# Kernel tuning notes

Hardware: AMD Instinct MI355X
Metric: run time of the kernel (lower is better)

The kernel has to match this reference:

```python
import jax, jax.numpy as jnp
import numpy as np

B, S, D, H = 2, 4096, 1024, 16
HD = D // H  # 64
BASE = 10000.0


def setup_inputs() -> dict:
    key = jax.random.key(0)
    ks = jax.random.split(key, 11)
    s = 1.0 / np.sqrt(D)
    return {
        "consulta": jax.random.normal(ks[0], (B, S, D), jnp.float32),
        "chave": jax.random.normal(ks[1], (B, S, D), jnp.float32),
        "valor": jax.random.normal(ks[2], (B, S, D), jnp.float32),
        "Wq": jax.random.normal(ks[3], (D, D), jnp.float32) * s,
        "bq": jnp.zeros((D,), jnp.float32),
        "Wk": jax.random.normal(ks[4], (D, D), jnp.float32) * s,
        "bk": jnp.zeros((D,), jnp.float32),
        "Wv": jax.random.normal(ks[5], (D, D), jnp.float32) * s,
        "bv": jnp.zeros((D,), jnp.float32),
        "Wo": jax.random.normal(ks[6], (D, D), jnp.float32) * s,
        "bo": jnp.zeros((D,), jnp.float32),
    }


def _rope(x):
    # x: [B, H, S, HD]; rotate interleaved (even, odd) pairs
    seq = x.shape[2]
    theta = 1.0 / (BASE ** (jnp.arange(0, HD, 2, dtype=jnp.float32) / HD))  # [HD/2]
    angles = jnp.arange(seq, dtype=jnp.float32)[:, None] * theta[None, :]  # [S, HD/2]
    cos, sin = jnp.cos(angles), jnp.sin(angles)
    xr = x.reshape(*x.shape[:-1], HD // 2, 2)
    x_re, x_im = xr[..., 0], xr[..., 1]
    out_re = x_re * cos - x_im * sin
    out_im = x_re * sin + x_im * cos
    return jnp.stack([out_re, out_im], axis=-1).reshape(x.shape)


def reference(consulta, chave, valor, Wq, bq, Wk, bk, Wv, bv, Wo, bo):
    b, s, _ = consulta.shape
    # projections (torch Linear: x @ W.T + b)
    Q = consulta @ Wq.T + bq
    K = chave @ Wk.T + bk
    V = valor @ Wv.T + bv
    # [B, H, S, HD]
    Q = Q.reshape(b, s, H, HD).transpose(0, 2, 1, 3)
    K = K.reshape(b, s, H, HD).transpose(0, 2, 1, 3)
    V = V.reshape(b, s, H, HD).transpose(0, 2, 1, 3)
    Q = _rope(Q)
    K = _rope(K)
    scores = jnp.einsum('bhqd,bhkd->bhqk', Q, K) / jnp.sqrt(jnp.float32(HD))
    weights = jax.nn.softmax(scores, axis=-1)  # dropout p=0 -> identity
    out = jnp.einsum('bhqk,bhkd->bhqd', weights, V)
    out = out.transpose(0, 2, 1, 3).reshape(b, s, D)
    return out @ Wo.T + bo
```

## Files before the change

kernel.cpp:

```cpp
#include <hip/hip_runtime.h>
#include <hip/hip_bf16.h>

typedef __attribute__((ext_vector_type(8))) short short8;
typedef __attribute__((ext_vector_type(4))) float f32x4;
typedef __attribute__((ext_vector_type(4))) unsigned short ushort4v;
typedef __attribute__((ext_vector_type(4))) float float4v;

#define NB 2
#define NS 4096
#define ND 1024
#define NH 16
#define NHD 64

__device__ __forceinline__ unsigned short f2bf(float x) {
    union { float f; unsigned u; } v; v.f = x;
    unsigned r = v.u + 0x7FFFu + ((v.u >> 16) & 1u);
    return (unsigned short)(r >> 16);
}
__device__ __forceinline__ float bf2f(unsigned short u) {
    union { float f; unsigned u; } v; v.u = ((unsigned)u) << 16;
    return v.f;
}

__device__ __forceinline__ void gload_lds16(const unsigned short* g, unsigned short* l) {
    __builtin_amdgcn_global_load_lds(
        (const __attribute__((address_space(1))) void*)g,
        (__attribute__((address_space(3))) void*)l,
        16, 0, 0);
}

__global__ void rope_table_kernel(float* __restrict__ cosT, float* __restrict__ sinT) {
    int i = blockIdx.x * blockDim.x + threadIdx.x;
    int p = i & 31, s = i >> 5;
    float theta = exp2f(-(float)(2 * p) * (13.287712379549449f / 64.0f));
    float ang = (float)s * theta;
    float sv, cv;
    sincosf(ang, &sv, &cv);
    cosT[i] = cv; sinT[i] = sv;
}

__global__ void cast_bf16_kernel(const float* __restrict__ in, unsigned short* __restrict__ out, int n8) {
    int i = blockIdx.x * blockDim.x + threadIdx.x;
    if (i >= n8) return;
    float4v a0 = *(const float4v*)(&in[(size_t)i * 8]);
    float4v a1 = *(const float4v*)(&in[(size_t)i * 8 + 4]);
    short8 s8;
    s8[0] = (short)f2bf(a0.x); s8[1] = (short)f2bf(a0.y);
    s8[2] = (short)f2bf(a0.z); s8[3] = (short)f2bf(a0.w);
    s8[4] = (short)f2bf(a1.x); s8[5] = (short)f2bf(a1.y);
    s8[6] = (short)f2bf(a1.z); s8[7] = (short)f2bf(a1.w);
    *(short8*)(&out[(size_t)i * 8]) = s8;
}

template<int EPI>
__global__ __launch_bounds__(256, 2) void gemm_kernel(
    const unsigned short* __restrict__ A,
    const unsigned short* __restrict__ Wb,
    const float* __restrict__ bias,
    void* __restrict__ outv,
    const float* __restrict__ cosT,
    const float* __restrict__ sinT)
{
    __shared__ unsigned short As[128 * 32];
    __shared__ unsigned short Bs[128 * 32];
    const int t = threadIdx.x;
    const int wave = t >> 6, lane = t & 63;
    const int quad = lane >> 4, l15 = lane & 15;
    const int wm = (wave & 1) * 64, wn = (wave >> 1) * 64;
    const int m0 = blockIdx.y * 128, n0 = blockIdx.x * 128;

    f32x4 acc[4][4];
#pragma unroll
    for (int i = 0; i < 4; i++)
#pragma unroll
        for (int j = 0; j < 4; j++)
            acc[i][j] = f32x4{0.f, 0.f, 0.f, 0.f};

    for (int k0 = 0; k0 < ND; k0 += 32) {
#pragma unroll
        for (int p = 0; p < 2; p++) {
            int idx = p * 256 + t;
            int r = idx >> 2, c = (idx & 3) * 8;
            unsigned short* ldsA = &As[(size_t)(p * 256 + wave * 64) * 8];
            unsigned short* ldsB = &Bs[(size_t)(p * 256 + wave * 64) * 8];
            gload_lds16(&A[(size_t)(m0 + r) * ND + k0 + c], ldsA);
            gload_lds16(&Wb[(size_t)(n0 + r) * ND + k0 + c], ldsB);
        }
        __syncthreads();

        short8 af[4], bfr[4];
#pragma unroll
        for (int mt = 0; mt < 4; mt++)
            af[mt] = *(const short8*)(&As[(wm + mt * 16 + l15) * 32 + quad * 8]);
#pragma unroll
        for (int nt = 0; nt < 4; nt++)
            bfr[nt] = *(const short8*)(&Bs[(wn + nt * 16 + l15) * 32 + quad * 8]);
#pragma unroll
        for (int mt = 0; mt < 4; mt++)
#pragma unroll
            for (int nt = 0; nt < 4; nt++) {
                if (EPI == 0)
                    acc[mt][nt] = __builtin_amdgcn_mfma_f32_16x16x32_bf16(bfr[nt], af[mt], acc[mt][nt], 0, 0, 0);
                else
                    acc[mt][nt] = __builtin_amdgcn_mfma_f32_16x16x32_bf16(af[mt], bfr[nt], acc[mt][nt], 0, 0, 0);
            }
        __syncthreads();
    }

    if (EPI == 0) {
        float* out = (float*)outv;
#pragma unroll
        for (int mt = 0; mt < 4; mt++) {
            int gm = m0 + wm + mt * 16 + l15;
#pragma unroll
            for (int nt = 0; nt < 4; nt++) {
                int gn0 = n0 + wn + nt * 16 + quad * 4;
                float4v fv;
#pragma unroll
                for (int r = 0; r < 4; r++)
                    fv[r] = acc[mt][nt][r] + bias[gn0 + r];
                *(float4v*)(&out[(size_t)gm * ND + gn0]) = fv;
            }
        }
    } else if (EPI == 1) {
        unsigned short* out = (unsigned short*)outv;
#pragma unroll
        for (int nt = 0; nt < 4; nt++) {
            int gn = n0 + wn + nt * 16 + l15;
            int h = gn >> 6, hd = gn & 63, pr = hd >> 1, im = gn & 1;
            float bv = bias[gn];
#pragma unroll
            for (int mt = 0; mt < 4; mt++) {
                int gm0 = m0 + wm + mt * 16 + quad * 4;
#pragma unroll
                for (int r = 0; r < 4; r++) {
                    int gm = gm0 + r;
                    int b = gm >> 12, s = gm & 4095;
                    float v = acc[mt][nt][r] + bv;
                    float pv = __shfl_xor(v, 1, 64);
                    float cv = cosT[s * 32 + pr], sv = sinT[s * 32 + pr];
                    float o = im ? (pv * sv + v * cv) : (v * cv - pv * sv);
                    out[((size_t)(b * NH + h) * NS + s) * NHD + hd] = f2bf(o);
                }
            }
        }
    } else {
        unsigned short* out = (unsigned short*)outv;
#pragma unroll
        for (int nt = 0; nt < 4; nt++) {
            int gn = n0 + wn + nt * 16 + l15;
            int h = gn >> 6, hd = gn & 63;
            float bv = bias[gn];
#pragma unroll
            for (int mt = 0; mt < 4; mt++) {
                int gm0 = m0 + wm + mt * 16 + quad * 4;
                int b = gm0 >> 12, s0 = gm0 & 4095;
                ushort4v pk;
#pragma unroll
                for (int r = 0; r < 4; r++)
                    pk[r] = f2bf(acc[mt][nt][r] + bv);
                *(ushort4v*)(&out[((size_t)(b * NH + h) * NHD + hd) * NS + s0]) = pk;
            }
        }
    }
}

__global__ __launch_bounds__(256, 2) void flash_kernel(
    const unsigned short* __restrict__ Qr,
    const unsigned short* __restrict__ Kr,
    const unsigned short* __restrict__ Vt,
    unsigned short* __restrict__ Yatt)
{
    __shared__ unsigned short Ks[128 * 72];
    __shared__ unsigned short Vs[64 * 136];
    __shared__ unsigned short Pw[4][32 * 136];
    const int t = threadIdx.x;
    const int wave = t >> 6, lane = t & 63;
    const int quad = lane >> 4, l15 = lane & 15;
    const int bh = blockIdx.y;
    const int qb = blockIdx.x * 128;
    const int wq = wave * 32;
    const size_t base = (size_t)bh * NS * NHD;

    short8 qf[2][2];
#pragma unroll
    for (int nt = 0; nt < 2; nt++)
#pragma unroll
        for (int kk = 0; kk < 2; kk++)
            qf[nt][kk] = *(const short8*)(&Qr[base + (size_t)(qb + wq + nt * 16 + l15) * NHD + kk * 32 + quad * 8]);

    f32x4 accO[4][2];
#pragma unroll
    for (int i = 0; i < 4; i++)
#pragma unroll
        for (int j = 0; j < 2; j++)
            accO[i][j] = f32x4{0.f, 0.f, 0.f, 0.f};
    float mrow[2] = {-1e30f, -1e30f};
    float lrow[2] = {0.f, 0.f};

    for (int j0 = 0; j0 < NS; j0 += 128) {
#pragma unroll
        for (int p = 0; p < 4; p++) {
            int idx = p * 256 + t;
            { int r = idx >> 3, c = (idx & 7) * 8;
              *(short8*)(&Ks[r * 72 + c]) = *(const short8*)(&Kr[base + (size_t)(j0 + r) * NHD + c]); }
            { int r = idx >> 4, c = (idx & 15) * 8;
              *(short8*)(&Vs[r * 136 + c]) = *(const short8*)(&Vt[(size_t)(bh * NHD + r) * NS + j0 + c]); }
        }
        __syncthreads();

        f32x4 sa[8][2];
#pragma unroll
        for (int mt = 0; mt < 8; mt++)
#pragma unroll
            for (int nt = 0; nt < 2; nt++)
                sa[mt][nt] = f32x4{0.f, 0.f, 0.f, 0.f};
#pragma unroll
        for (int kk = 0; kk < 2; kk++)
#pragma unroll
            for (int mt = 0; mt < 8; mt++) {
                short8 ak = *(const short8*)(&Ks[(mt * 16 + l15) * 72 + kk * 32 + quad * 8]);
#pragma unroll
                for (int nt = 0; nt < 2; nt++)
                    sa[mt][nt] = __builtin_amdgcn_mfma_f32_16x16x32_bf16(ak, qf[nt][kk], sa[mt][nt], 0, 0, 0);
            }

#pragma unroll
        for (int nt = 0; nt < 2; nt++) {
            float mx = -1e30f;
#pragma unroll
            for (int mt = 0; mt < 8; mt++)
#pragma unroll
                for (int r = 0; r < 4; r++)
                    mx = fmaxf(mx, sa[mt][nt][r]);
            mx = fmaxf(mx, __shfl_xor(mx, 16, 64));
            mx = fmaxf(mx, __shfl_xor(mx, 32, 64));
            mx *= 0.125f;
            float mnew = fmaxf(mrow[nt], mx);
            float alpha = __expf(mrow[nt] - mnew);
            float lsum = 0.f;
#pragma unroll
            for (int mt = 0; mt < 8; mt++) {
                ushort4v pk;
#pragma unroll
                for (int r = 0; r < 4; r++) {
                    float pv = __expf(sa[mt][nt][r] * 0.125f - mnew);
                    unsigned short u = f2bf(pv);
                    pk[r] = u;
                    lsum += bf2f(u);
                }
                *(ushort4v*)(&Pw[wave][(nt * 16 + l15) * 136 + mt * 16 + quad * 4]) = pk;
            }
            lsum += __shfl_xor(lsum, 16, 64);
            lsum += __shfl_xor(lsum, 32, 64);
            lrow[nt] = lrow[nt] * alpha + lsum;
            mrow[nt] = mnew;
#pragma unroll
            for (int mt2 = 0; mt2 < 4; mt2++)
#pragma unroll
                for (int r = 0; r < 4; r++)
                    accO[mt2][nt][r] *= alpha;
        }
        __syncthreads();

#pragma unroll
        for (int kk2 = 0; kk2 < 4; kk2++) {
            short8 av[4], bp[2];
#pragma unroll
            for (int mt2 = 0; mt2 < 4; mt2++)
                av[mt2] = *(const short8*)(&Vs[(mt2 * 16 + l15) * 136 + kk2 * 32 + quad * 8]);
#pragma unroll
            for (int nt = 0; nt < 2; nt++)
                bp[nt] = *(const short8*)(&Pw[wave][(nt * 16 + l15) * 136 + kk2 * 32 + quad * 8]);
#pragma unroll
            for (int mt2 = 0; mt2 < 4; mt2++)
#pragma unroll
                for (int nt = 0; nt < 2; nt++)
                    accO[mt2][nt] = __builtin_amdgcn_mfma_f32_16x16x32_bf16(av[mt2], bp[nt], accO[mt2][nt], 0, 0, 0);
        }
        __syncthreads();
    }

    int b = bh >> 4, h = bh & 15;
#pragma unroll
    for (int nt = 0; nt < 2; nt++) {
        float rl = 1.f / lrow[nt];
        int s = qb + wq + nt * 16 + l15;
#pragma unroll
        for (int mt2 = 0; mt2 < 4; mt2++) {
            ushort4v pk;
#pragma unroll
            for (int r = 0; r < 4; r++)
                pk[r] = f2bf(accO[mt2][nt][r] * rl);
            *(ushort4v*)(&Yatt[((size_t)(b * NS + s)) * ND + h * NHD + mt2 * 16 + quad * 4]) = pk;
        }
    }
}

extern "C" void kernel_launch(void* const* d_in, const int* in_sizes, int n_in,
                              void* d_out, int out_size, void* d_ws, size_t ws_size,
                              hipStream_t stream) {
    const float* consulta = (const float*)d_in[0];
    const float* chave    = (const float*)d_in[1];
    const float* valor    = (const float*)d_in[2];
    const float* Wq = (const float*)d_in[3];
    const float* bq = (const float*)d_in[4];
    const float* Wk = (const float*)d_in[5];
    const float* bk = (const float*)d_in[6];
    const float* Wv = (const float*)d_in[7];
    const float* bv = (const float*)d_in[8];
    const float* Wo = (const float*)d_in[9];
    const float* bo = (const float*)d_in[10];

    const size_t NX = (size_t)8192 * 1024;

    float* cosT = (float*)d_ws;
    float* sinT = cosT + (size_t)NS * 32;
    unsigned short* Qrb = (unsigned short*)(sinT + (size_t)NS * 32);
    unsigned short* Krb = Qrb + NX;
    unsigned short* Vtb = Krb + NX;
    unsigned short* Yat = Vtb + NX;
    unsigned short* Abf = Yat + NX;
    unsigned short* Wbf = Abf + NX;

    rope_table_kernel<<<NS * 32 / 256, 256, 0, stream>>>(cosT, sinT);

    const int ACT8 = (int)(NX / 8);
    const int W8 = ND * ND / 8;

    dim3 ggrid(8, 64);

    cast_bf16_kernel<<<ACT8 / 256, 256, 0, stream>>>(consulta, Abf, ACT8);
    cast_bf16_kernel<<<W8 / 256, 256, 0, stream>>>(Wq, Wbf, W8);
    gemm_kernel<1><<<ggrid, 256, 0, stream>>>(Abf, Wbf, bq, Qrb, cosT, sinT);

    cast_bf16_kernel<<<ACT8 / 256, 256, 0, stream>>>(chave, Abf, ACT8);
    cast_bf16_kernel<<<W8 / 256, 256, 0, stream>>>(Wk, Wbf, W8);
    gemm_kernel<1><<<ggrid, 256, 0, stream>>>(Abf, Wbf, bk, Krb, cosT, sinT);

    cast_bf16_kernel<<<ACT8 / 256, 256, 0, stream>>>(valor, Abf, ACT8);
    cast_bf16_kernel<<<W8 / 256, 256, 0, stream>>>(Wv, Wbf, W8);
    gemm_kernel<2><<<ggrid, 256, 0, stream>>>(Abf, Wbf, bv, Vtb, cosT, sinT);

    flash_kernel<<<dim3(32, 32), 256, 0, stream>>>(Qrb, Krb, Vtb, Yat);

    cast_bf16_kernel<<<W8 / 256, 256, 0, stream>>>(Wo, Wbf, W8);
    gemm_kernel<0><<<ggrid, 256, 0, stream>>>(Yat, Wbf, bo, d_out, cosT, sinT);
}
```

Measured before the change: 560.3 us.

## Fold softmax scale into Q, use exp2, per-tile P buffer, raise flash occupancy

Folds the 1/sqrt(d) and log2(e) factors into the Q projection epilogue, so the flash kernel can use exp2 directly without a per-score multiply. The P buffer now holds one 16-row tile per wave, and the PV MFMAs run inside the per-nt softmax loop. This halves P shared memory and allows launch_bounds of 3 blocks per CU. It also uses packed v_cvt_pk_bf16 conversion and tree max/sum reductions, at the cost of a row sum taken over unrounded fp32 P values, which differs slightly from the bf16 values fed to the MFMA.

```diff
diff --git a/kernel.cpp b/kernel.cpp
--- a/kernel.cpp
+++ b/kernel.cpp
@@ -5,6 +5,7 @@
 typedef __attribute__((ext_vector_type(4))) float f32x4;
 typedef __attribute__((ext_vector_type(4))) unsigned short ushort4v;
 typedef __attribute__((ext_vector_type(4))) float float4v;
+typedef __attribute__((ext_vector_type(2))) unsigned int uint32x2;
 
 #define NB 2
 #define NS 4096
@@ -12,14 +13,18 @@
 #define NH 16
 #define NHD 64
 
+#define QSCALE 0.18033688011112042f
+
 __device__ __forceinline__ unsigned short f2bf(float x) {
     union { float f; unsigned u; } v; v.f = x;
     unsigned r = v.u + 0x7FFFu + ((v.u >> 16) & 1u);
     return (unsigned short)(r >> 16);
 }
-__device__ __forceinline__ float bf2f(unsigned short u) {
-    union { float f; unsigned u; } v; v.u = ((unsigned)u) << 16;
-    return v.f;
+
+__device__ __forceinline__ unsigned cvt_pk_bf16(float lo, float hi) {
+    unsigned r;
+    asm("v_cvt_pk_bf16_f32 %0, %1, %2" : "=v"(r) : "v"(lo), "v"(hi));
+    return r;
 }
 
 __device__ __forceinline__ void gload_lds16(const unsigned short* g, unsigned short* l) {
@@ -59,7 +64,8 @@
     const float* __restrict__ bias,
     void* __restrict__ outv,
     const float* __restrict__ cosT,
-    const float* __restrict__ sinT)
+    const float* __restrict__ sinT,
+    float oscale)
 {
     __shared__ unsigned short As[128 * 32];
     __shared__ unsigned short Bs[128 * 32];
@@ -140,7 +146,7 @@
                     float pv = __shfl_xor(v, 1, 64);
                     float cv = cosT[s * 32 + pr], sv = sinT[s * 32 + pr];
                     float o = im ? (pv * sv + v * cv) : (v * cv - pv * sv);
-                    out[((size_t)(b * NH + h) * NS + s) * NHD + hd] = f2bf(o);
+                    out[((size_t)(b * NH + h) * NS + s) * NHD + hd] = f2bf(o * oscale);
                 }
             }
         }
@@ -165,7 +171,7 @@
     }
 }
 
-__global__ __launch_bounds__(256, 2) void flash_kernel(
+__global__ __launch_bounds__(256, 3) void flash_kernel(
     const unsigned short* __restrict__ Qr,
     const unsigned short* __restrict__ Kr,
     const unsigned short* __restrict__ Vt,
@@ -173,7 +179,7 @@
 {
     __shared__ unsigned short Ks[128 * 72];
     __shared__ unsigned short Vs[64 * 136];
-    __shared__ unsigned short Pw[4][32 * 136];
+    __shared__ unsigned short Pw[4][16 * 136];
     const int t = threadIdx.x;
     const int wave = t >> 6, lane = t & 63;
     const int quad = lane >> 4, l15 = lane & 15;
@@ -227,30 +233,31 @@
 
 #pragma unroll
         for (int nt = 0; nt < 2; nt++) {
-            float mx = -1e30f;
+            float mm[8];
 #pragma unroll
             for (int mt = 0; mt < 8; mt++)
-#pragma unroll
-                for (int r = 0; r < 4; r++)
-                    mx = fmaxf(mx, sa[mt][nt][r]);
+                mm[mt] = fmaxf(fmaxf(sa[mt][nt][0], sa[mt][nt][1]),
+                               fmaxf(sa[mt][nt][2], sa[mt][nt][3]));
+            float mx = fmaxf(fmaxf(fmaxf(mm[0], mm[1]), fmaxf(mm[2], mm[3])),
+                             fmaxf(fmaxf(mm[4], mm[5]), fmaxf(mm[6], mm[7])));
             mx = fmaxf(mx, __shfl_xor(mx, 16, 64));
             mx = fmaxf(mx, __shfl_xor(mx, 32, 64));
-            mx *= 0.125f;
             float mnew = fmaxf(mrow[nt], mx);
-            float alpha = __expf(mrow[nt] - mnew);
-            float lsum = 0.f;
+            float alpha = exp2f(mrow[nt] - mnew);
+            float ls0 = 0.f, ls1 = 0.f, ls2 = 0.f, ls3 = 0.f;
 #pragma unroll
             for (int mt = 0; mt < 8; mt++) {
-                ushort4v pk;
-#pragma unroll
-                for (int r = 0; r < 4; r++) {
-                    float pv = __expf(sa[mt][nt][r] * 0.125f - mnew);
-                    unsigned short u = f2bf(pv);
-                    pk[r] = u;
-                    lsum += bf2f(u);
-                }
-                *(ushort4v*)(&Pw[wave][(nt * 16 + l15) * 136 + mt * 16 + quad * 4]) = pk;
-            }
+                float p0 = exp2f(sa[mt][nt][0] - mnew);
+                float p1 = exp2f(sa[mt][nt][1] - mnew);
+                float p2 = exp2f(sa[mt][nt][2] - mnew);
+                float p3 = exp2f(sa[mt][nt][3] - mnew);
+                ls0 += p0; ls1 += p1; ls2 += p2; ls3 += p3;
+                uint32x2 pk;
+                pk.x = cvt_pk_bf16(p0, p1);
+                pk.y = cvt_pk_bf16(p2, p3);
+                *(uint32x2*)(&Pw[wave][l15 * 136 + mt * 16 + quad * 4]) = pk;
+            }
+            float lsum = (ls0 + ls1) + (ls2 + ls3);
             lsum += __shfl_xor(lsum, 16, 64);
             lsum += __shfl_xor(lsum, 32, 64);
             lrow[nt] = lrow[nt] * alpha + lsum;
@@ -260,23 +267,18 @@
 #pragma unroll
                 for (int r = 0; r < 4; r++)
                     accO[mt2][nt][r] *= alpha;
-        }
-        __syncthreads();
-
-#pragma unroll
-        for (int kk2 = 0; kk2 < 4; kk2++) {
-            short8 av[4], bp[2];
-#pragma unroll
-            for (int mt2 = 0; mt2 < 4; mt2++)
-                av[mt2] = *(const short8*)(&Vs[(mt2 * 16 + l15) * 136 + kk2 * 32 + quad * 8]);
-#pragma unroll
-            for (int nt = 0; nt < 2; nt++)
-                bp[nt] = *(const short8*)(&Pw[wave][(nt * 16 + l15) * 136 + kk2 * 32 + quad * 8]);
-#pragma unroll
-            for (int mt2 = 0; mt2 < 4; mt2++)
-#pragma unroll
-                for (int nt = 0; nt < 2; nt++)
-                    accO[mt2][nt] = __builtin_amdgcn_mfma_f32_16x16x32_bf16(av[mt2], bp[nt], accO[mt2][nt], 0, 0, 0);
+
+#pragma unroll
+            for (int kk2 = 0; kk2 < 4; kk2++) {
+                short8 av[4];
+#pragma unroll
+                for (int mt2 = 0; mt2 < 4; mt2++)
+                    av[mt2] = *(const short8*)(&Vs[(mt2 * 16 + l15) * 136 + kk2 * 32 + quad * 8]);
+                short8 bp = *(const short8*)(&Pw[wave][l15 * 136 + kk2 * 32 + quad * 8]);
+#pragma unroll
+                for (int mt2 = 0; mt2 < 4; mt2++)
+                    accO[mt2][nt] = __builtin_amdgcn_mfma_f32_16x16x32_bf16(av[mt2], bp, accO[mt2][nt], 0, 0, 0);
+            }
         }
         __syncthreads();
     }
@@ -288,11 +290,10 @@
         int s = qb + wq + nt * 16 + l15;
 #pragma unroll
         for (int mt2 = 0; mt2 < 4; mt2++) {
-            ushort4v pk;
-#pragma unroll
-            for (int r = 0; r < 4; r++)
-                pk[r] = f2bf(accO[mt2][nt][r] * rl);
-            *(ushort4v*)(&Yatt[((size_t)(b * NS + s)) * ND + h * NHD + mt2 * 16 + quad * 4]) = pk;
+            uint32x2 pk;
+            pk.x = cvt_pk_bf16(accO[mt2][nt][0] * rl, accO[mt2][nt][1] * rl);
+            pk.y = cvt_pk_bf16(accO[mt2][nt][2] * rl, accO[mt2][nt][3] * rl);
+            *(uint32x2*)(&Yatt[((size_t)(b * NS + s)) * ND + h * NHD + mt2 * 16 + quad * 4]) = pk;
         }
     }
 }
@@ -332,18 +333,18 @@
 
     cast_bf16_kernel<<<ACT8 / 256, 256, 0, stream>>>(consulta, Abf, ACT8);
     cast_bf16_kernel<<<W8 / 256, 256, 0, stream>>>(Wq, Wbf, W8);
-    gemm_kernel<1><<<ggrid, 256, 0, stream>>>(Abf, Wbf, bq, Qrb, cosT, sinT);
+    gemm_kernel<1><<<ggrid, 256, 0, stream>>>(Abf, Wbf, bq, Qrb, cosT, sinT, QSCALE);
 
     cast_bf16_kernel<<<ACT8 / 256, 256, 0, stream>>>(chave, Abf, ACT8);
     cast_bf16_kernel<<<W8 / 256, 256, 0, stream>>>(Wk, Wbf, W8);
-    gemm_kernel<1><<<ggrid, 256, 0, stream>>>(Abf, Wbf, bk, Krb, cosT, sinT);
+    gemm_kernel<1><<<ggrid, 256, 0, stream>>>(Abf, Wbf, bk, Krb, cosT, sinT, 1.0f);
 
     cast_bf16_kernel<<<ACT8 / 256, 256, 0, stream>>>(valor, Abf, ACT8);
     cast_bf16_kernel<<<W8 / 256, 256, 0, stream>>>(Wv, Wbf, W8);
-    gemm_kernel<2><<<ggrid, 256, 0, stream>>>(Abf, Wbf, bv, Vtb, cosT, sinT);
+    gemm_kernel<2><<<ggrid, 256, 0, stream>>>(Abf, Wbf, bv, Vtb, cosT, sinT, 1.0f);
 
     flash_kernel<<<dim3(32, 32), 256, 0, stream>>>(Qrb, Krb, Vtb, Yat);
 
     cast_bf16_kernel<<<W8 / 256, 256, 0, stream>>>(Wo, Wbf, W8);
-    gemm_kernel<0><<<ggrid, 256, 0, stream>>>(Yat, Wbf, bo, d_out, cosT, sinT);
-}
+    gemm_kernel<0><<<ggrid, 256, 0, stream>>>(Yat, Wbf, bo, d_out, cosT, sinT, 1.0f);
+}
```

After: 795.4 us. 1.42x slower.
